# Optimization experiments

Hardware: AMD Instinct MI355X
Metric: run time of the kernel (lower is better)

Reference implementation:

```python
import jax, jax.numpy as jnp
from jax import lax
import numpy as np

VOCAB = 50000
E = 301  # 300-dim pretrained + appended ones column
D = 25
NUM_CLASSES = 5


def setup_inputs() -> dict:
    key = jax.random.key(0)
    ks = jax.random.split(key, 8)
    B, S = 2048, 128
    words = jax.random.randint(ks[0], (B, S), 0, VOCAB)
    emb = jax.random.normal(ks[1], (VOCAB, E - 1), dtype=jnp.float32)
    # hstack ones column as in __init__
    emb_table = jnp.concatenate([emb, jnp.ones((VOCAB, 1), jnp.float32)], axis=1)
    A = jax.random.normal(ks[2], (D, E, D), dtype=jnp.float32) * 0.02
    W = jax.random.normal(ks[3], (E, D), dtype=jnp.float32) * 0.02
    V = jax.random.normal(ks[4], (D, D), dtype=jnp.float32) * 0.02
    b = jax.random.normal(ks[5], (D,), dtype=jnp.float32) * 0.02
    out_W = jax.random.normal(ks[6], (NUM_CLASSES, D), dtype=jnp.float32) * 0.02
    out_b = jax.random.normal(ks[7], (NUM_CLASSES,), dtype=jnp.float32) * 0.02
    return {"words": words, "batch_size": B, "emb_table": emb_table,
            "A": A, "W": W, "V": V, "b": b, "out_W": out_W, "out_b": out_b}


def reference(words, batch_size, emb_table, A, W, V, b, out_W, out_b):
    x_seq = emb_table[words]                      # [B, S, E] frozen embedding gather
    h0 = jnp.zeros((batch_size, D), jnp.float32).at[:, -1].set(1.0)

    def step(h, x):  # x: [B, E], h: [B, D]
        # a[b,i] = sum_{e,j} x[b,e] A[i,e,j] h[b,j]  (bilinear tensor term)
        a = jnp.einsum('be,ied,bd->bi', x, A, h)
        lin = x @ W + h @ V + b
        return jnp.tanh(a + lin), None

    h, _ = lax.scan(step, h0, jnp.swapaxes(x_seq, 0, 1))  # scan over S
    logits = h @ out_W.T + out_b                 # [B, num_classes]
    return jax.nn.sigmoid(logits)
```

## Files before the change

kernel.cpp:

```cpp
#include <hip/hip_runtime.h>
#include <math.h>

#define VOCAB 50000
#define EE 301
#define KP 304
#define DD 25
#define SEQ 128
#define NC 5
#define BROW 768
#define NUSE 700
#define TROW 704
#define EMT 50048

#define GLOAD_LDS16(g, l) __builtin_amdgcn_global_load_lds( \
    (const __attribute__((address_space(1))) void*)(g),     \
    (__attribute__((address_space(3))) void*)(l), 16, 0, 0)

__global__ __launch_bounds__(256) void build_B(
    const float* __restrict__ A, const float* __restrict__ W,
    float* __restrict__ Bmat)
{
    int e = blockIdx.x;
    for (int c = threadIdx.x; c < BROW; c += 256) {
        float v = 0.f;
        if (e < EE && c < NUSE) {
            int i = c / 28, j = c % 28;
            if (j < 25)       v = A[((size_t)i * EE + e) * DD + j];
            else if (j == 25) v = W[(size_t)e * DD + i];
        }
        Bmat[(size_t)e * BROW + c] = v;
    }
}

__global__ __launch_bounds__(256) void transpose_emb(
    const float* __restrict__ emb, float* __restrict__ embT)
{
    __shared__ float t[64][65];
    int m0 = blockIdx.x * 64, k0 = blockIdx.y * 64;
    int tx = threadIdx.x & 63, ty = threadIdx.x >> 6;
#pragma unroll
    for (int it = 0; it < 16; ++it) {
        int m = m0 + ty * 16 + it;
        int k = k0 + tx;
        t[tx][ty * 16 + it] = (m < VOCAB && k < EE) ? emb[(size_t)m * EE + k] : 0.f;
    }
    __syncthreads();
#pragma unroll
    for (int it = 0; it < 16; ++it) {
        int kl = ty * 16 + it;
        int k = k0 + kl;
        if (k < KP) embT[(size_t)k * EMT + m0 + tx] = t[kl][tx];
    }
}

__global__ __launch_bounds__(256, 1) void gemm_T3(
    const float* __restrict__ embT,
    const float* __restrict__ Bmat,
    float* __restrict__ T)
{
    __shared__ float As[2][16][128];
    __shared__ float Bs[2][16][256];
    int tid = threadIdx.x;
    int tx = tid & 15, ty = tid >> 4;
    int m0 = blockIdx.x * 128, n0 = blockIdx.y * 256;
    int wave = tid >> 6, lane = tid & 63;
    int krow = lane >> 5;
    int col4 = (lane & 31) * 4;

    float acc[8][16];
#pragma unroll
    for (int a = 0; a < 8; ++a)
#pragma unroll
        for (int c = 0; c < 16; ++c) acc[a][c] = 0.f;

    auto dma_tile = [&](int k0, int buf) {
#pragma unroll
        for (int j = 0; j < 2; ++j) {
            int r0 = wave * 4 + j * 2;
            int k = k0 + r0 + krow;
            GLOAD_LDS16(embT + (size_t)k * EMT + m0 + col4, &As[buf][r0][0]);
        }
#pragma unroll
        for (int j = 0; j < 4; ++j) {
            int r = wave * 4 + j;
            int k = k0 + r;
            GLOAD_LDS16(Bmat + (size_t)k * BROW + n0 + lane * 4, &Bs[buf][r][0]);
        }
    };

    dma_tile(0, 0);
    __syncthreads();

    int buf = 0;
    for (int k0 = 0; k0 < KP; k0 += 16) {
        if (k0 + 16 < KP) dma_tile(k0 + 16, buf ^ 1);
#pragma unroll
        for (int kk = 0; kk < 16; ++kk) {
            float4 a0 = *(const float4*)&As[buf][kk][ty * 4];
            float4 a1 = *(const float4*)&As[buf][kk][64 + ty * 4];
            float4 b0 = *(const float4*)&Bs[buf][kk][tx * 4];
            float4 b1 = *(const float4*)&Bs[buf][kk][64 + tx * 4];
            float4 b2 = *(const float4*)&Bs[buf][kk][128 + tx * 4];
            float4 b3 = *(const float4*)&Bs[buf][kk][192 + tx * 4];
            float av[8]  = {a0.x, a0.y, a0.z, a0.w, a1.x, a1.y, a1.z, a1.w};
            float bv[16] = {b0.x, b0.y, b0.z, b0.w, b1.x, b1.y, b1.z, b1.w,
                            b2.x, b2.y, b2.z, b2.w, b3.x, b3.y, b3.z, b3.w};
#pragma unroll
            for (int a = 0; a < 8; ++a)
#pragma unroll
                for (int c = 0; c < 16; ++c)
                    acc[a][c] = fmaf(av[a], bv[c], acc[a][c]);
        }
        __syncthreads();
        buf ^= 1;
    }

#pragma unroll
    for (int gi = 0; gi < 2; ++gi) {
#pragma unroll
        for (int r = 0; r < 4; ++r) {
            int m = m0 + gi * 64 + ty * 4 + r;
            if (m < VOCAB) {
                float* row = T + (size_t)m * TROW;
#pragma unroll
                for (int gc = 0; gc < 4; ++gc) {
                    int n = n0 + gc * 64 + tx * 4;
                    if (n < TROW) {
                        int a = gi * 4 + r, c = gc * 4;
                        *(float4*)(row + n) = make_float4(
                            acc[a][c], acc[a][c + 1], acc[a][c + 2], acc[a][c + 3]);
                    }
                }
            }
        }
    }
}

__global__ __launch_bounds__(256, 2) void gemm_T(
    const float* __restrict__ emb, const float* __restrict__ Bmat,
    float* __restrict__ T)
{
    __shared__ float As[2][16][132];
    __shared__ float Bs[2][16][132];
    int tid = threadIdx.x;
    int tx = tid & 15, ty = tid >> 4;
    int m0 = blockIdx.x * 128, n0 = blockIdx.y * 128;
    float acc[8][8];
#pragma unroll
    for (int a = 0; a < 8; ++a)
#pragma unroll
        for (int c = 0; c < 8; ++c) acc[a][c] = 0.f;
    float ar[8]; float4 br[2];
    int kl0 = tid >> 5, nl0 = (tid & 31) * 4;
#pragma unroll
    for (int it = 0; it < 8; ++it) {
        int m = m0 + ty + 16 * it, k = tx;
        ar[it] = (m < VOCAB && k < EE) ? emb[(size_t)m * EE + k] : 0.f;
    }
#pragma unroll
    for (int it = 0; it < 2; ++it) {
        int k = kl0 + 8 * it;
        br[it] = (k < EE) ? *(const float4*)(Bmat + (size_t)k * BROW + n0 + nl0)
                          : make_float4(0.f, 0.f, 0.f, 0.f);
    }
#pragma unroll
    for (int it = 0; it < 8; ++it) As[0][tx][ty + 16 * it] = ar[it];
#pragma unroll
    for (int it = 0; it < 2; ++it) *(float4*)(&Bs[0][kl0 + 8 * it][nl0]) = br[it];
    __syncthreads();
    int buf = 0;
    for (int k0 = 0; k0 < EE; k0 += 16) {
        int k1 = k0 + 16;
        bool more = (k1 < EE);
        if (more) {
#pragma unroll
            for (int it = 0; it < 8; ++it) {
                int m = m0 + ty + 16 * it, k = k1 + tx;
                ar[it] = (m < VOCAB && k < EE) ? emb[(size_t)m * EE + k] : 0.f;
            }
#pragma unroll
            for (int it = 0; it < 2; ++it) {
                int k = k1 + kl0 + 8 * it;
                br[it] = (k < EE) ? *(const float4*)(Bmat + (size_t)k * BROW + n0 + nl0)
                                  : make_float4(0.f, 0.f, 0.f, 0.f);
            }
        }
#pragma unroll
        for (int kk = 0; kk < 16; ++kk) {
            float4 a0 = *(const float4*)&As[buf][kk][ty * 4];
            float4 a1 = *(const float4*)&As[buf][kk][64 + ty * 4];
            float4 b0 = *(const float4*)&Bs[buf][kk][tx * 4];
            float4 b1 = *(const float4*)&Bs[buf][kk][64 + tx * 4];
            float av[8] = {a0.x, a0.y, a0.z, a0.w, a1.x, a1.y, a1.z, a1.w};
            float bv[8] = {b0.x, b0.y, b0.z, b0.w, b1.x, b1.y, b1.z, b1.w};
#pragma unroll
            for (int a = 0; a < 8; ++a)
#pragma unroll
                for (int c = 0; c < 8; ++c)
                    acc[a][c] = fmaf(av[a], bv[c], acc[a][c]);
        }
        if (more) {
            int nb = buf ^ 1;
#pragma unroll
            for (int it = 0; it < 8; ++it) As[nb][tx][ty + 16 * it] = ar[it];
#pragma unroll
            for (int it = 0; it < 2; ++it) *(float4*)(&Bs[nb][kl0 + 8 * it][nl0]) = br[it];
            __syncthreads();
            buf = nb;
        }
    }
#pragma unroll
    for (int gi = 0; gi < 2; ++gi) {
#pragma unroll
        for (int r = 0; r < 4; ++r) {
            int m = m0 + gi * 64 + ty * 4 + r;
            if (m < VOCAB) {
                float* row = T + (size_t)m * TROW;
#pragma unroll
                for (int gc = 0; gc < 2; ++gc) {
                    int n = n0 + gc * 64 + tx * 4;
                    if (n < TROW) {
                        int a = gi * 4 + r, c = gc * 4;
                        *(float4*)(row + n) = make_float4(
                            acc[a][c], acc[a][c + 1], acc[a][c + 2], acc[a][c + 3]);
                    }
                }
            }
        }
    }
}

__global__ __launch_bounds__(256, 1) void rnn_scan_np6(
    const int*   __restrict__ words,
    const float* __restrict__ T,
    const float* __restrict__ V,
    const float* __restrict__ bvec,
    const float* __restrict__ outW,
    const float* __restrict__ outB,
    float* __restrict__ out,
    int B)
{
    int tid = threadIdx.x;
    int g = tid >> 5, i = tid & 31;
    int b = blockIdx.x * 8 + g;
    bool act = (i < DD) && (b < B);
    int ii = (i < DD) ? i : (DD - 1);
    int bsafe = (b < B) ? b : 0;
    const int* wr = words + (size_t)bsafe * SEQ;

    float Vcol[DD];
#pragma unroll
    for (int j = 0; j < DD; ++j) Vcol[j] = V[j * DD + ii];
    float bi = bvec[ii];

    float hr[DD];
#pragma unroll
    for (int j = 0; j < DD; ++j) hr[j] = 0.f;
    hr[DD - 1] = 1.f;

    bool sse = ((b & 3) == 0) && ((i & 3) == 0);
    const float* base = T + (size_t)ii * 28;

    float4 A0[7], A1[7], A2[7], A3[7];
    auto LD = [&](float4* dst, int t) {
        const float* R = base + (size_t)wr[t] * TROW;
#pragma unroll
        for (int u = 0; u < 7; ++u) dst[u] = *(const float4*)(R + u * 4);
    };

    float hnew = 0.f;
    auto STEP = [&](const float4* C) {
        float Tj[28];
#pragma unroll
        for (int u = 0; u < 7; ++u) {
            Tj[u * 4 + 0] = C[u].x; Tj[u * 4 + 1] = C[u].y;
            Tj[u * 4 + 2] = C[u].z; Tj[u * 4 + 3] = C[u].w;
        }
        float qv = Tj[25];
        float a;
        if (sse) {
            float p0 = 0.f, p1 = 0.f, p2 = 0.f, p3 = 0.f;
#pragma unroll
            for (int j = 0; j < 24; j += 4) {
                p0 = __fadd_rn(p0, __fmul_rn(Tj[j],     hr[j]));
                p1 = __fadd_rn(p1, __fmul_rn(Tj[j + 1], hr[j + 1]));
                p2 = __fadd_rn(p2, __fmul_rn(Tj[j + 2], hr[j + 2]));
                p3 = __fadd_rn(p3, __fmul_rn(Tj[j + 3], hr[j + 3]));
            }
            float s02 = __fadd_rn(p0, p2);
            float s13 = __fadd_rn(p1, p3);
            a = __fadd_rn(s02, s13);
            a = __fadd_rn(a, __fmul_rn(Tj[24], hr[24]));
        } else {
            a = 0.f;
#pragma unroll
            for (int j = 0; j < DD; ++j)
                a = __fadd_rn(a, __fmul_rn(Tj[j], hr[j]));
        }
        float r2 = 0.f;
#pragma unroll
        for (int j = 0; j < DD; ++j)
            r2 = fmaf(hr[j], Vcol[j], r2);
        float lin = __fadd_rn(__fadd_rn(qv, r2), bi);
        float pre = __fadd_rn(a, lin);
        hnew = act ? (float)tanh((double)pre) : 0.f;
#pragma unroll
        for (int j = 0; j < DD; ++j)
            hr[j] = __shfl(hnew, j, 32);
    };

    LD(A0, 0); LD(A1, 1); LD(A2, 2);
    int t = 0;
    for (; t + 6 < SEQ; t += 4) {
        LD(A3, t + 3); STEP(A0);
        LD(A0, t + 4); STEP(A1);
        LD(A1, t + 5); STEP(A2);
        LD(A2, t + 6); STEP(A3);
    }
    LD(A3, 127);
    STEP(A0); STEP(A1); STEP(A2); STEP(A3);

    if (i < NC && b < B) {
        float acc = 0.f;
#pragma unroll
        for (int j = 0; j < DD; ++j)
            acc = fmaf(hr[j], outW[i * DD + j], acc);
        float l = __fadd_rn(acc, outB[i]);
        out[(size_t)b * NC + i] = (float)(1.0 / (1.0 + exp(-(double)l)));
    }
}

extern "C" void kernel_launch(void* const* d_in, const int* in_sizes, int n_in,
                              void* d_out, int out_size, void* d_ws, size_t ws_size,
                              hipStream_t stream)
{
    const int*   words = (const int*)d_in[0];
    const float* emb   = (const float*)d_in[2];
    const float* A     = (const float*)d_in[3];
    const float* W     = (const float*)d_in[4];
    const float* V     = (const float*)d_in[5];
    const float* bias  = (const float*)d_in[6];
    const float* outW  = (const float*)d_in[7];
    const float* outB  = (const float*)d_in[8];
    float* out = (float*)d_out;
    int B = in_sizes[0] / SEQ;

    const size_t T_OFF    = (size_t)1 << 20;
    const size_t EMBT_OFF = (size_t)144 << 20;
    const size_t NEED     = EMBT_OFF + (size_t)KP * EMT * 4;
    float* Bmat = (float*)d_ws;
    float* T    = (float*)((char*)d_ws + T_OFF);
    float* embT = (float*)((char*)d_ws + EMBT_OFF);

    build_B<<<KP, 256, 0, stream>>>(A, W, Bmat);
    if (ws_size >= NEED) {
        transpose_emb<<<dim3(EMT / 64, (KP + 63) / 64), 256, 0, stream>>>(emb, embT);
        gemm_T3<<<dim3((VOCAB + 127) / 128, 3), 256, 0, stream>>>(embT, Bmat, T);
    } else {
        gemm_T<<<dim3((VOCAB + 127) / 128, 6), 256, 0, stream>>>(emb, Bmat, T);
    }
    rnn_scan_np6<<<(B + 7) / 8, 256, 0, stream>>>(words, T, V, bias, outW, outB, out, B);
}
```

Measured before the change: 502.4 us.

## Use persistent 160-row GEMM tiles with grid-stride scheduling and 2 blocks/CU

The vocab-projection GEMM now uses 160-row M tiles with a 10x16 register micro-tile per thread, so each B tile load is amortised over more rows. A fixed grid of 512 persistent blocks walks all tiles in grid-stride order, and launch bounds ask for two blocks per CU. The embedding transpose is padded to 50112 columns to fit whole 160-row tiles. The larger accumulator raises register pressure, which could limit occupancy or cause spills at the 2-block target.

```diff
diff --git a/kernel.cpp b/kernel.cpp
--- a/kernel.cpp
+++ b/kernel.cpp
@@ -10,7 +10,11 @@
 #define BROW 768
 #define NUSE 700
 #define TROW 704
-#define EMT 50048
+#define EMT 50112
+#define TM 160
+#define MTILES 313
+#define NTILES (MTILES*3)
+#define GEMM_GRID 512
 
 #define GLOAD_LDS16(g, l) __builtin_amdgcn_global_load_lds( \
     (const __attribute__((address_space(1))) void*)(g),     \
@@ -53,80 +57,96 @@
     }
 }
 
-__global__ __launch_bounds__(256, 1) void gemm_T3(
+__global__ __launch_bounds__(256, 2) void gemm_T5(
     const float* __restrict__ embT,
     const float* __restrict__ Bmat,
     float* __restrict__ T)
 {
-    __shared__ float As[2][16][128];
+    __shared__ float As[2][16 * TM];
     __shared__ float Bs[2][16][256];
     int tid = threadIdx.x;
     int tx = tid & 15, ty = tid >> 4;
-    int m0 = blockIdx.x * 128, n0 = blockIdx.y * 256;
     int wave = tid >> 6, lane = tid & 63;
-    int krow = lane >> 5;
-    int col4 = (lane & 31) * 4;
-
-    float acc[8][16];
-#pragma unroll
-    for (int a = 0; a < 8; ++a)
-#pragma unroll
-        for (int c = 0; c < 16; ++c) acc[a][c] = 0.f;
-
-    auto dma_tile = [&](int k0, int buf) {
-#pragma unroll
-        for (int j = 0; j < 2; ++j) {
-            int r0 = wave * 4 + j * 2;
-            int k = k0 + r0 + krow;
-            GLOAD_LDS16(embT + (size_t)k * EMT + m0 + col4, &As[buf][r0][0]);
-        }
-#pragma unroll
-        for (int j = 0; j < 4; ++j) {
-            int r = wave * 4 + j;
-            int k = k0 + r;
-            GLOAD_LDS16(Bmat + (size_t)k * BROW + n0 + lane * 4, &Bs[buf][r][0]);
-        }
-    };
-
-    dma_tile(0, 0);
-    __syncthreads();
-
-    int buf = 0;
-    for (int k0 = 0; k0 < KP; k0 += 16) {
-        if (k0 + 16 < KP) dma_tile(k0 + 16, buf ^ 1);
-#pragma unroll
-        for (int kk = 0; kk < 16; ++kk) {
-            float4 a0 = *(const float4*)&As[buf][kk][ty * 4];
-            float4 a1 = *(const float4*)&As[buf][kk][64 + ty * 4];
-            float4 b0 = *(const float4*)&Bs[buf][kk][tx * 4];
-            float4 b1 = *(const float4*)&Bs[buf][kk][64 + tx * 4];
-            float4 b2 = *(const float4*)&Bs[buf][kk][128 + tx * 4];
-            float4 b3 = *(const float4*)&Bs[buf][kk][192 + tx * 4];
-            float av[8]  = {a0.x, a0.y, a0.z, a0.w, a1.x, a1.y, a1.z, a1.w};
-            float bv[16] = {b0.x, b0.y, b0.z, b0.w, b1.x, b1.y, b1.z, b1.w,
-                            b2.x, b2.y, b2.z, b2.w, b3.x, b3.y, b3.z, b3.w};
-#pragma unroll
-            for (int a = 0; a < 8; ++a)
-#pragma unroll
-                for (int c = 0; c < 16; ++c)
-                    acc[a][c] = fmaf(av[a], bv[c], acc[a][c]);
-        }
+
+    int aoff[3], alds[3]; bool aval[3];
+#pragma unroll
+    for (int j = 0; j < 3; ++j) {
+        int t = j * 4 + wave;
+        aval[j] = (t < 10);
+        int f = (t < 10 ? t : 0) * 256 + lane * 4;
+        int kk = f / TM;
+        int col = f - kk * TM;
+        aoff[j] = kk * EMT + col;
+        alds[j] = (t < 10 ? t : 0) * 1024;
+    }
+
+    for (int tix = blockIdx.x; tix < NTILES; tix += gridDim.x) {
+        int mi = tix / 3, ni = tix - mi * 3;
+        int m0 = mi * TM, n0 = ni * 256;
+
+        float acc[10][16];
+#pragma unroll
+        for (int a = 0; a < 10; ++a)
+#pragma unroll
+            for (int c = 0; c < 16; ++c) acc[a][c] = 0.f;
+
+        auto dma_tile = [&](int k0, int buf) {
+#pragma unroll
+            for (int j = 0; j < 3; ++j)
+                if (aval[j])
+                    GLOAD_LDS16(embT + (size_t)k0 * EMT + m0 + aoff[j],
+                                (char*)&As[buf][0] + alds[j]);
+#pragma unroll
+            for (int j = 0; j < 4; ++j) {
+                int r = wave * 4 + j;
+                GLOAD_LDS16(Bmat + (size_t)(k0 + r) * BROW + n0 + lane * 4,
+                            &Bs[buf][r][0]);
+            }
+        };
+
+        dma_tile(0, 0);
         __syncthreads();
-        buf ^= 1;
-    }
-
-#pragma unroll
-    for (int gi = 0; gi < 2; ++gi) {
-#pragma unroll
-        for (int r = 0; r < 4; ++r) {
-            int m = m0 + gi * 64 + ty * 4 + r;
+
+        int buf = 0;
+        for (int k0 = 0; k0 < KP; k0 += 16) {
+            if (k0 + 16 < KP) dma_tile(k0 + 16, buf ^ 1);
+#pragma unroll
+            for (int kk = 0; kk < 16; ++kk) {
+                const float* Ar = &As[buf][kk * TM];
+                float4 a0 = *(const float4*)&Ar[ty * 4];
+                float4 a1 = *(const float4*)&Ar[64 + ty * 4];
+                float2 a2 = *(const float2*)&Ar[128 + ty * 2];
+                float4 b0 = *(const float4*)&Bs[buf][kk][tx * 4];
+                float4 b1 = *(const float4*)&Bs[buf][kk][64 + tx * 4];
+                float4 b2 = *(const float4*)&Bs[buf][kk][128 + tx * 4];
+                float4 b3 = *(const float4*)&Bs[buf][kk][192 + tx * 4];
+                float av[10] = {a0.x, a0.y, a0.z, a0.w, a1.x, a1.y, a1.z, a1.w,
+                                a2.x, a2.y};
+                float bv[16] = {b0.x, b0.y, b0.z, b0.w, b1.x, b1.y, b1.z, b1.w,
+                                b2.x, b2.y, b2.z, b2.w, b3.x, b3.y, b3.z, b3.w};
+#pragma unroll
+                for (int a = 0; a < 10; ++a)
+#pragma unroll
+                    for (int c = 0; c < 16; ++c)
+                        acc[a][c] = fmaf(av[a], bv[c], acc[a][c]);
+            }
+            __syncthreads();
+            buf ^= 1;
+        }
+
+#pragma unroll
+        for (int a = 0; a < 10; ++a) {
+            int mo = (a < 4) ? (ty * 4 + a)
+                   : (a < 8) ? (64 + ty * 4 + (a - 4))
+                             : (128 + ty * 2 + (a - 8));
+            int m = m0 + mo;
             if (m < VOCAB) {
                 float* row = T + (size_t)m * TROW;
 #pragma unroll
                 for (int gc = 0; gc < 4; ++gc) {
                     int n = n0 + gc * 64 + tx * 4;
                     if (n < TROW) {
-                        int a = gi * 4 + r, c = gc * 4;
+                        int c = gc * 4;
                         *(float4*)(row + n) = make_float4(
                             acc[a][c], acc[a][c + 1], acc[a][c + 2], acc[a][c + 3]);
                     }
@@ -355,7 +375,7 @@
     build_B<<<KP, 256, 0, stream>>>(A, W, Bmat);
     if (ws_size >= NEED) {
         transpose_emb<<<dim3(EMT / 64, (KP + 63) / 64), 256, 0, stream>>>(emb, embT);
-        gemm_T3<<<dim3((VOCAB + 127) / 128, 3), 256, 0, stream>>>(embT, Bmat, T);
+        gemm_T5<<<GEMM_GRID, 256, 0, stream>>>(embT, Bmat, T);
     } else {
         gemm_T<<<dim3((VOCAB + 127) / 128, 6), 256, 0, stream>>>(emb, Bmat, T);
     }
```

After: 1.431 ms. 185% more time.

## Use persistent GEMM grid with split tail tiles for load balance

Applied to the files above, without the earlier changes.

Replaces the 391x3 one-block-per-tile GEMM launch with a persistent 512-block grid that loops over 128x256 tiles, then splits the remaining tail tiles into 128x128 halves so the last wave is better balanced across CUs. EMT is padded to 50112 so the extra M tile reads stay in bounds. This targets wave-quantization idle time in the final round of tiles, at the cost of extra loop overhead and a second code path.

```diff
diff --git a/kernel.cpp b/kernel.cpp
--- a/kernel.cpp
+++ b/kernel.cpp
@@ -10,7 +10,12 @@
 #define BROW 768
 #define NUSE 700
 #define TROW 704
-#define EMT 50048
+#define EMT 50112
+#define MTILES 391
+#define NTILES (MTILES*3)
+#define FULLT 1024
+#define SUBT ((NTILES - FULLT) * 2)
+#define GEMM_GRID 512
 
 #define GLOAD_LDS16(g, l) __builtin_amdgcn_global_load_lds( \
     (const __attribute__((address_space(1))) void*)(g),     \
@@ -53,82 +58,157 @@
     }
 }
 
-__global__ __launch_bounds__(256, 1) void gemm_T3(
+__global__ __launch_bounds__(256, 1) void gemm_T6(
     const float* __restrict__ embT,
     const float* __restrict__ Bmat,
     float* __restrict__ T)
 {
-    __shared__ float As[2][16][128];
-    __shared__ float Bs[2][16][256];
+    __shared__ float As[2][16 * 128];
+    __shared__ float Bs[2][16 * 256];
     int tid = threadIdx.x;
     int tx = tid & 15, ty = tid >> 4;
-    int m0 = blockIdx.x * 128, n0 = blockIdx.y * 256;
     int wave = tid >> 6, lane = tid & 63;
     int krow = lane >> 5;
     int col4 = (lane & 31) * 4;
 
     float acc[8][16];
-#pragma unroll
-    for (int a = 0; a < 8; ++a)
-#pragma unroll
-        for (int c = 0; c < 16; ++c) acc[a][c] = 0.f;
-
-    auto dma_tile = [&](int k0, int buf) {
-#pragma unroll
-        for (int j = 0; j < 2; ++j) {
-            int r0 = wave * 4 + j * 2;
-            int k = k0 + r0 + krow;
-            GLOAD_LDS16(embT + (size_t)k * EMT + m0 + col4, &As[buf][r0][0]);
-        }
-#pragma unroll
-        for (int j = 0; j < 4; ++j) {
-            int r = wave * 4 + j;
-            int k = k0 + r;
-            GLOAD_LDS16(Bmat + (size_t)k * BROW + n0 + lane * 4, &Bs[buf][r][0]);
-        }
-    };
-
-    dma_tile(0, 0);
-    __syncthreads();
-
-    int buf = 0;
-    for (int k0 = 0; k0 < KP; k0 += 16) {
-        if (k0 + 16 < KP) dma_tile(k0 + 16, buf ^ 1);
-#pragma unroll
-        for (int kk = 0; kk < 16; ++kk) {
-            float4 a0 = *(const float4*)&As[buf][kk][ty * 4];
-            float4 a1 = *(const float4*)&As[buf][kk][64 + ty * 4];
-            float4 b0 = *(const float4*)&Bs[buf][kk][tx * 4];
-            float4 b1 = *(const float4*)&Bs[buf][kk][64 + tx * 4];
-            float4 b2 = *(const float4*)&Bs[buf][kk][128 + tx * 4];
-            float4 b3 = *(const float4*)&Bs[buf][kk][192 + tx * 4];
-            float av[8]  = {a0.x, a0.y, a0.z, a0.w, a1.x, a1.y, a1.z, a1.w};
-            float bv[16] = {b0.x, b0.y, b0.z, b0.w, b1.x, b1.y, b1.z, b1.w,
-                            b2.x, b2.y, b2.z, b2.w, b3.x, b3.y, b3.z, b3.w};
-#pragma unroll
-            for (int a = 0; a < 8; ++a)
-#pragma unroll
-                for (int c = 0; c < 16; ++c)
-                    acc[a][c] = fmaf(av[a], bv[c], acc[a][c]);
-        }
+
+    for (int t = blockIdx.x; t < FULLT; t += gridDim.x) {
+        int mi = t / 3, ni = t - mi * 3;
+        int m0 = mi * 128, n0 = ni * 256;
+
+#pragma unroll
+        for (int a = 0; a < 8; ++a)
+#pragma unroll
+            for (int c = 0; c < 16; ++c) acc[a][c] = 0.f;
+
+        auto dma_tile = [&](int k0, int buf) {
+#pragma unroll
+            for (int j = 0; j < 2; ++j) {
+                int r0 = wave * 4 + j * 2;
+                int k = k0 + r0 + krow;
+                GLOAD_LDS16(embT + (size_t)k * EMT + m0 + col4, &As[buf][r0 * 128]);
+            }
+#pragma unroll
+            for (int j = 0; j < 4; ++j) {
+                int r = wave * 4 + j;
+                GLOAD_LDS16(Bmat + (size_t)(k0 + r) * BROW + n0 + lane * 4,
+                            &Bs[buf][r * 256]);
+            }
+        };
+
+        dma_tile(0, 0);
         __syncthreads();
-        buf ^= 1;
-    }
-
-#pragma unroll
-    for (int gi = 0; gi < 2; ++gi) {
-#pragma unroll
-        for (int r = 0; r < 4; ++r) {
-            int m = m0 + gi * 64 + ty * 4 + r;
-            if (m < VOCAB) {
-                float* row = T + (size_t)m * TROW;
-#pragma unroll
-                for (int gc = 0; gc < 4; ++gc) {
-                    int n = n0 + gc * 64 + tx * 4;
-                    if (n < TROW) {
-                        int a = gi * 4 + r, c = gc * 4;
-                        *(float4*)(row + n) = make_float4(
-                            acc[a][c], acc[a][c + 1], acc[a][c + 2], acc[a][c + 3]);
+
+        int buf = 0;
+        for (int k0 = 0; k0 < KP; k0 += 16) {
+            if (k0 + 16 < KP) dma_tile(k0 + 16, buf ^ 1);
+#pragma unroll
+            for (int kk = 0; kk < 16; ++kk) {
+                const float* Ar = &As[buf][kk * 128];
+                const float* Br = &Bs[buf][kk * 256];
+                float4 a0 = *(const float4*)&Ar[ty * 4];
+                float4 a1 = *(const float4*)&Ar[64 + ty * 4];
+                float4 b0 = *(const float4*)&Br[tx * 4];
+                float4 b1 = *(const float4*)&Br[64 + tx * 4];
+                float4 b2 = *(const float4*)&Br[128 + tx * 4];
+                float4 b3 = *(const float4*)&Br[192 + tx * 4];
+                float av[8]  = {a0.x, a0.y, a0.z, a0.w, a1.x, a1.y, a1.z, a1.w};
+                float bv[16] = {b0.x, b0.y, b0.z, b0.w, b1.x, b1.y, b1.z, b1.w,
+                                b2.x, b2.y, b2.z, b2.w, b3.x, b3.y, b3.z, b3.w};
+#pragma unroll
+                for (int a = 0; a < 8; ++a)
+#pragma unroll
+                    for (int c = 0; c < 16; ++c)
+                        acc[a][c] = fmaf(av[a], bv[c], acc[a][c]);
+            }
+            __syncthreads();
+            buf ^= 1;
+        }
+
+#pragma unroll
+        for (int gi = 0; gi < 2; ++gi) {
+#pragma unroll
+            for (int r = 0; r < 4; ++r) {
+                int m = m0 + gi * 64 + ty * 4 + r;
+                if (m < VOCAB) {
+                    float* row = T + (size_t)m * TROW;
+#pragma unroll
+                    for (int gc = 0; gc < 4; ++gc) {
+                        int n = n0 + gc * 64 + tx * 4;
+                        if (n < TROW) {
+                            int a = gi * 4 + r, c = gc * 4;
+                            *(float4*)(row + n) = make_float4(
+                                acc[a][c], acc[a][c + 1], acc[a][c + 2], acc[a][c + 3]);
+                        }
+                    }
+                }
+            }
+        }
+    }
+
+    for (int s = blockIdx.x; s < SUBT; s += gridDim.x) {
+        int p   = FULLT + (s >> 1);
+        int sub = s & 1;
+        int mi = p / 3, ni = p - mi * 3;
+        int m0 = mi * 128, n0 = ni * 256 + sub * 128;
+
+#pragma unroll
+        for (int a = 0; a < 8; ++a)
+#pragma unroll
+            for (int c = 0; c < 8; ++c) acc[a][c] = 0.f;
+
+        auto dma_sub = [&](int k0, int buf) {
+#pragma unroll
+            for (int j = 0; j < 2; ++j) {
+                int r0 = wave * 4 + j * 2;
+                int k = k0 + r0 + krow;
+                GLOAD_LDS16(embT + (size_t)k * EMT + m0 + col4, &As[buf][r0 * 128]);
+                GLOAD_LDS16(Bmat + (size_t)k * BROW + n0 + col4, &Bs[buf][r0 * 128]);
+            }
+        };
+
+        dma_sub(0, 0);
+        __syncthreads();
+
+        int buf = 0;
+        for (int k0 = 0; k0 < KP; k0 += 16) {
+            if (k0 + 16 < KP) dma_sub(k0 + 16, buf ^ 1);
+#pragma unroll
+            for (int kk = 0; kk < 16; ++kk) {
+                const float* Ar = &As[buf][kk * 128];
+                const float* Br = &Bs[buf][kk * 128];
+                float4 a0 = *(const float4*)&Ar[ty * 4];
+                float4 a1 = *(const float4*)&Ar[64 + ty * 4];
+                float4 b0 = *(const float4*)&Br[tx * 4];
+                float4 b1 = *(const float4*)&Br[64 + tx * 4];
+                float av[8] = {a0.x, a0.y, a0.z, a0.w, a1.x, a1.y, a1.z, a1.w};
+                float bv[8] = {b0.x, b0.y, b0.z, b0.w, b1.x, b1.y, b1.z, b1.w};
+#pragma unroll
+                for (int a = 0; a < 8; ++a)
+#pragma unroll
+                    for (int c = 0; c < 8; ++c)
+                        acc[a][c] = fmaf(av[a], bv[c], acc[a][c]);
+            }
+            __syncthreads();
+            buf ^= 1;
+        }
+
+#pragma unroll
+        for (int gi = 0; gi < 2; ++gi) {
+#pragma unroll
+            for (int r = 0; r < 4; ++r) {
+                int m = m0 + gi * 64 + ty * 4 + r;
+                if (m < VOCAB) {
+                    float* row = T + (size_t)m * TROW;
+#pragma unroll
+                    for (int gc = 0; gc < 2; ++gc) {
+                        int n = n0 + gc * 64 + tx * 4;
+                        if (n < TROW) {
+                            int a = gi * 4 + r, c = gc * 4;
+                            *(float4*)(row + n) = make_float4(
+                                acc[a][c], acc[a][c + 1], acc[a][c + 2], acc[a][c + 3]);
+                        }
                     }
                 }
             }
@@ -355,7 +435,7 @@
     build_B<<<KP, 256, 0, stream>>>(A, W, Bmat);
     if (ws_size >= NEED) {
         transpose_emb<<<dim3(EMT / 64, (KP + 63) / 64), 256, 0, stream>>>(emb, embT);
-        gemm_T3<<<dim3((VOCAB + 127) / 128, 3), 256, 0, stream>>>(embT, Bmat, T);
+        gemm_T6<<<GEMM_GRID, 256, 0, stream>>>(embT, Bmat, T);
     } else {
         gemm_T<<<dim3((VOCAB + 127) / 128, 6), 256, 0, stream>>>(emb, Bmat, T);
     }
```

After: 626.5 us. 1.25x slower.
